# Kernel optimization log

Hardware: AMD Instinct MI355X
Metric: run time of the kernel (lower is better)

## Reference

```python
import jax, jax.numpy as jnp
import numpy as np

# ---- config (matches init_kwargs) ----
B, CIN, IMG = 4, 3, 129
PATCH, STRIDE, PAD = 4, 1, 1
DIM = CIN * PATCH * PATCH          # 48, Token_performer input dim
EMB = 256                          # out_channel -> in_dim -> emb
M = EMB // 2                       # kernel_ratio=0.5 random features
UP = 2                             # up_scale
EPS = 1e-8


def layernorm(x, g, b):
    mu = x.mean(-1, keepdims=True)
    var = ((x - mu) ** 2).mean(-1, keepdims=True)
    return (x - mu) / jnp.sqrt(var + 1e-5) * g + b


def unfold(x, k=PATCH, pad=PAD):
    # torch nn.Unfold, stride=1: output [B, C*k*k, L*L], channel order (c, kh, kw)
    Bs, C, H, W = x.shape
    xp = jnp.pad(x, ((0, 0), (0, 0), (pad, pad), (pad, pad)))
    L = H + 2 * pad - k + 1
    cols = jnp.stack([xp[:, :, i:i + L, j:j + L]
                      for i in range(k) for j in range(k)], axis=2)  # [B,C,k*k,L,L]
    return cols.reshape(Bs, C * k * k, L * L)


def prm_exp(x, w):
    # Performer positive random features: exp(w@x - |x|^2/2)/sqrt(m)
    xd = 0.5 * jnp.sum(x * x, axis=-1, keepdims=True)          # [B,T,1]
    wtx = jnp.einsum('btd,md->btm', x, w)                       # [B,T,M]
    return jnp.exp(wtx - xd) / jnp.sqrt(jnp.float32(w.shape[0]))


def upsample_bilinear_ac(x, scale):
    # nn.UpsamplingBilinear2d => align_corners=True
    Bs, C, H, W = x.shape
    Ho, Wo = H * scale, W * scale
    def coords(n_in, n_out):
        f = jnp.arange(n_out, dtype=jnp.float32) * (n_in - 1) / (n_out - 1)
        i0 = jnp.clip(jnp.floor(f).astype(jnp.int32), 0, n_in - 2)
        return i0, f - i0.astype(jnp.float32)
    h0, th = coords(H, Ho)
    w0, tw = coords(W, Wo)
    xh = x[:, :, h0, :] * (1 - th)[None, None, :, None] + x[:, :, h0 + 1, :] * th[None, None, :, None]
    return xh[:, :, :, w0] * (1 - tw) + xh[:, :, :, w0 + 1] * tw


def setup_inputs() -> dict:
    key = jax.random.key(0)
    ks = jax.random.split(key, 8)
    def n(k, shape, s=0.02):
        return jax.random.normal(k, shape, dtype=jnp.float32) * s
    return dict(
        x=jax.random.normal(ks[0], (B, CIN, IMG, IMG), dtype=jnp.float32),
        g1=jnp.ones((DIM,), jnp.float32), b1=jnp.zeros((DIM,), jnp.float32),
        w_kqv=n(ks[1], (DIM, 3 * EMB)), b_kqv=jnp.zeros((3 * EMB,), jnp.float32),
        w_prm=jax.random.normal(ks[2], (M, EMB), dtype=jnp.float32) * 0.7,  # ~ orthogonal*sqrt(m)
        w_proj=n(ks[3], (EMB, EMB)), b_proj=jnp.zeros((EMB,), jnp.float32),
        g2=jnp.ones((EMB,), jnp.float32), b2=jnp.zeros((EMB,), jnp.float32),
        w_mlp1=n(ks[4], (EMB, EMB)), b_mlp1=jnp.zeros((EMB,), jnp.float32),
        w_mlp2=n(ks[5], (EMB, EMB)), b_mlp2=jnp.zeros((EMB,), jnp.float32),
    )


def reference(x, g1, b1, w_kqv, b_kqv, w_prm, w_proj, b_proj, g2, b2,
              w_mlp1, b_mlp1, w_mlp2, b_mlp2):
    Bs = x.shape[0]
    t = unfold(x).transpose(0, 2, 1)                     # [B, T, DIM], T = 128*128
    h = layernorm(t, g1, b1)
    kqv = h @ w_kqv + b_kqv                              # [B, T, 3*EMB]
    k, q, v = jnp.split(kqv, 3, axis=-1)                 # torch split order: k, q, v
    kp, qp = prm_exp(k, w_prm), prm_exp(q, w_prm)        # [B, T, M]
    D = jnp.einsum('btm,bm->bt', qp, kp.sum(axis=1))[..., None]   # [B,T,1]
    kptv = jnp.einsum('btn,btm->bnm', v, kp)             # [B, EMB, M]
    y = jnp.einsum('btm,bnm->btn', qp, kptv) / (D + EPS) # [B, T, EMB]
    y = v + (y @ w_proj + b_proj)                        # skip uses v
    z = layernorm(y, g2, b2)
    y = y + (jax.nn.gelu(z @ w_mlp1 + b_mlp1, approximate=False) @ w_mlp2 + b_mlp2)
    T = y.shape[1]
    S = int(np.sqrt(T))
    img = y.transpose(0, 2, 1).reshape(Bs, EMB, S, S)    # [B, 256, 128, 128]
    return upsample_bilinear_ac(img, UP)                 # [B, 256, 256, 256]
```

## Files before the change

### kernel.cpp

```cpp
#include <hip/hip_runtime.h>
#include <math.h>

#define TOK   16384
#define DIM   48
#define EMB   256
#define MF    128
#define IMGsz 129

typedef __attribute__((ext_vector_type(8))) short    bf16x8;
typedef __attribute__((ext_vector_type(8))) unsigned short u16x8;
typedef __attribute__((ext_vector_type(4))) float    f32x4;

__device__ __forceinline__ ushort f2bf(float f) {
    union { float f; unsigned u; } v; v.f = f;
    unsigned u = v.u;
    return (ushort)((u + 0x7fffu + ((u >> 16) & 1u)) >> 16);
}
__device__ __forceinline__ float bf2f(ushort h) {
    union { unsigned u; float f; } v; v.u = ((unsigned)h) << 16; return v.f;
}

#define SWZ512(r,c) ((r)*512 + (((((c)>>3) ^ ((r)&7))) << 3) + ((c)&7))
#define SWZ64(r,c)  ((r)*64  + (((((c)>>3) ^ ((r)&7)) & 7) << 3) + ((c)&7))
#define SWZ256(r,c) ((r)*256 + (((((c)>>3) ^ ((r)&7))) << 3) + ((c)&7))

__device__ __forceinline__ int fragmajor(int n, int k, int KC) {
    return (((n >> 4)*KC + (k >> 5))*4 + ((k >> 3) & 3))*128 + (n & 15)*8 + (k & 7);
}

__global__ __launch_bounds__(256) void kprep(
    const float* __restrict__ w_kqv, const float* __restrict__ w_prm,
    const float* __restrict__ w_proj, const float* __restrict__ w_mlp1,
    const float* __restrict__ w_mlp2,
    ushort* __restrict__ wkqvT, ushort* __restrict__ wprm_bf, ushort* __restrict__ wT3)
{
    int blk = blockIdx.x, tid = threadIdx.x;
    if (blk < 768) {
        if (tid < 64) {
            float v = (tid < DIM) ? w_kqv[tid*768 + blk] : 0.f;
            wkqvT[fragmajor(blk, tid, 2)] = f2bf(v);
        }
    } else if (blk < 896) {
        int m = blk - 768;
        wprm_bf[fragmajor(m, tid, 8)] = f2bf(w_prm[m*256 + tid]);
    } else {
        int q = blk - 896;
        int w = q >> 8, n = q & 255;
        const float* src = (w == 0) ? w_proj : ((w == 1) ? w_mlp1 : w_mlp2);
        wT3[w*65536 + fragmajor(n, tid, 8)] = f2bf(src[tid*256 + n]);
    }
}

__global__ __launch_bounds__(256, 2) void k1_mfma(
    const float* __restrict__ x, const float* __restrict__ g1, const float* __restrict__ b1,
    const ushort* __restrict__ wkqvT, const float* __restrict__ b_kqv,
    const ushort* __restrict__ wprm_bf,
    ushort* __restrict__ vfrag_out, ushort* __restrict__ vT_out,
    ushort* __restrict__ kpT_out, ushort* __restrict__ qp_out)
{
    __shared__ __align__(16) ushort kq_bf[32*512];
    __shared__ __align__(16) ushort vt_bf[32*256];
    __shared__ float xdp[4][32][2];
    __shared__ float xd2[32][2];
    __shared__ float red1[32][8], red2[32][8];
    __shared__ float mu_s[32], iv_s[32];

    float*  t_s  = (float*)kq_bf;
    ushort* h_bf = vt_bf;

    const int blk = blockIdx.x;
    const int b  = blk >> 9;
    const int t0 = (blk & 511) << 5;
    const int tid = threadIdx.x;
    const int wid = tid >> 6;
    const int l15 = tid & 15, l4 = (tid >> 4) & 3;

    for (int e = tid; e < 32*DIM; e += 256) {
        int tok = e / DIM, j = e - tok*DIM;
        int t = t0 + tok;
        int lh = t >> 7, lw = t & 127;
        int c = j >> 4, kh = (j >> 2) & 3, kw = j & 3;
        int ih = lh + kh - 1, iw = lw + kw - 1;
        float val = 0.f;
        if (ih >= 0 && ih < IMGsz && iw >= 0 && iw < IMGsz)
            val = x[((b*3 + c)*IMGsz + ih)*IMGsz + iw];
        t_s[tok*DIM + j] = val;
    }
    __syncthreads();

    {
        int tg = tid >> 3, sl = tid & 7;
        const float* tr = &t_s[tg*DIM + sl*6];
        float s1 = 0.f, s2 = 0.f;
        #pragma unroll
        for (int j = 0; j < 6; j++) { float a = tr[j]; s1 += a; s2 = fmaf(a, a, s2); }
        red1[tg][sl] = s1; red2[tg][sl] = s2;
        __syncthreads();
        if (tid < 32) {
            float a = 0.f, q = 0.f;
            #pragma unroll
            for (int j = 0; j < 8; j++) { a += red1[tid][j]; q += red2[tid][j]; }
            float mu = a * (1.f/DIM);
            mu_s[tid] = mu;
            iv_s[tid] = rsqrtf(q*(1.f/DIM) - mu*mu + 1e-5f);
        }
        __syncthreads();
        float mu = mu_s[tg], iv = iv_s[tg];
        #pragma unroll
        for (int j = 0; j < 6; j++) {
            int c = sl*6 + j;
            h_bf[SWZ64(tg, c)] = f2bf((tr[j]-mu)*iv*g1[c] + b1[c]);
        }
        h_bf[SWZ64(tg, 48 + sl*2    )] = 0;
        h_bf[SWZ64(tg, 48 + sl*2 + 1)] = 0;
    }
    __syncthreads();

    f32x4 acc[2][12];
    #pragma unroll
    for (int m = 0; m < 2; m++)
        #pragma unroll
        for (int j = 0; j < 12; j++) { acc[m][j][0]=0.f; acc[m][j][1]=0.f; acc[m][j][2]=0.f; acc[m][j][3]=0.f; }
    #pragma unroll
    for (int kc = 0; kc < 2; kc++) {
        int ch = ((kc*4 + l4) ^ (l15 & 7)) << 3;
        bf16x8 a0 = *(const bf16x8*)&h_bf[ l15      *64 + ch];
        bf16x8 a1 = *(const bf16x8*)&h_bf[(16 + l15)*64 + ch];
        #pragma unroll
        for (int j = 0; j < 12; j++) {
            int ntile = wid + 4*j;
            bf16x8 bb = *(const bf16x8*)&wkqvT[(((ntile*2 + kc)*4 + l4)*16 + l15)*8];
            acc[0][j] = __builtin_amdgcn_mfma_f32_16x16x32_bf16(a0, bb, acc[0][j], 0, 0, 0);
            acc[1][j] = __builtin_amdgcn_mfma_f32_16x16x32_bf16(a1, bb, acc[1][j], 0, 0, 0);
        }
    }
    __syncthreads();

    {
        float pk[2][4], pq[2][4];
        #pragma unroll
        for (int m = 0; m < 2; m++)
            #pragma unroll
            for (int r = 0; r < 4; r++) { pk[m][r] = 0.f; pq[m][r] = 0.f; }
        #pragma unroll
        for (int j = 0; j < 12; j++) {
            int col = (wid + 4*j)*16 + l15;
            float bias = b_kqv[col];
            #pragma unroll
            for (int m = 0; m < 2; m++)
                #pragma unroll
                for (int r = 0; r < 4; r++) {
                    int row = m*16 + l4*4 + r;
                    float a = acc[m][j][r] + bias;
                    if (j < 4) {
                        pk[m][r] = fmaf(a, a, pk[m][r]);
                        kq_bf[SWZ512(row, col)] = f2bf(a);
                    } else if (j < 8) {
                        pq[m][r] = fmaf(a, a, pq[m][r]);
                        kq_bf[SWZ512(row, col)] = f2bf(a);
                    } else {
                        int n = col - 512;
                        vt_bf[row*256 + n] = f2bf(a);
                    }
                }
        }
        #pragma unroll
        for (int m = 0; m < 2; m++)
            #pragma unroll
            for (int r = 0; r < 4; r++) {
                float a = pk[m][r], q = pq[m][r];
                #pragma unroll
                for (int msk = 8; msk >= 1; msk >>= 1) {
                    a += __shfl_xor(a, msk);
                    q += __shfl_xor(q, msk);
                }
                if (l15 == 0) {
                    int row = m*16 + l4*4 + r;
                    xdp[wid][row][0] = a; xdp[wid][row][1] = q;
                }
            }
    }
    __syncthreads();
    if (tid < 64) {
        int row = tid >> 1, ty = tid & 1;
        xd2[row][ty] = 0.5f*(xdp[0][row][ty] + xdp[1][row][ty] + xdp[2][row][ty] + xdp[3][row][ty]);
    }

    {
        ushort* dst = vT_out + ((size_t)(b*EMB + tid))*TOK + t0;
        #pragma unroll
        for (int t8 = 0; t8 < 4; t8++) {
            u16x8 pk8;
            #pragma unroll
            for (int j = 0; j < 8; j++) pk8[j] = vt_bf[(t8*8 + j)*256 + tid];
            *(u16x8*)&dst[t8*8] = pk8;
        }
    }
    {
        u16x8 pk8[4];
        #pragma unroll
        for (int m = 0; m < 2; m++)
            #pragma unroll
            for (int nt = 0; nt < 4; nt++)
                #pragma unroll
                for (int r = 0; r < 4; r++) {
                    int row = m*16 + l4*4 + r;
                    int col = wid*64 + nt*16 + l15;
                    int idx = m*16 + nt*4 + r;
                    pk8[idx >> 3][idx & 7] = vt_bf[row*256 + col];
                }
        ushort* dst = vfrag_out + (size_t)blk*8192 + tid*32;
        #pragma unroll
        for (int i = 0; i < 4; i++) *(u16x8*)&dst[i*8] = pk8[i];
    }
    __syncthreads();

    f32x4 acc2[2][4];
    #pragma unroll
    for (int m = 0; m < 2; m++)
        #pragma unroll
        for (int n = 0; n < 4; n++) { acc2[m][n][0]=0.f; acc2[m][n][1]=0.f; acc2[m][n][2]=0.f; acc2[m][n][3]=0.f; }
    {
        const int cbase = (wid >= 2) ? 32 : 0;
        #pragma unroll
        for (int kc = 0; kc < 8; kc++) {
            int chunk = cbase + kc*4 + l4;
            int ch = (chunk ^ (l15 & 7)) << 3;
            bf16x8 a0 = *(const bf16x8*)&kq_bf[ l15      *512 + ch];
            bf16x8 a1 = *(const bf16x8*)&kq_bf[(16 + l15)*512 + ch];
            #pragma unroll
            for (int nt = 0; nt < 4; nt++) {
                int mtile = (wid & 1)*4 + nt;
                bf16x8 bb = *(const bf16x8*)&wprm_bf[(((mtile*8 + kc)*4 + l4)*16 + l15)*8];
                acc2[0][nt] = __builtin_amdgcn_mfma_f32_16x16x32_bf16(a0, bb, acc2[0][nt], 0, 0, 0);
                acc2[1][nt] = __builtin_amdgcn_mfma_f32_16x16x32_bf16(a1, bb, acc2[1][nt], 0, 0, 0);
            }
        }
    }

    {
        const float scale = 0.08838834764831845f;
        const bool isK = (wid < 2);
        #pragma unroll
        for (int m = 0; m < 2; m++)
            #pragma unroll
            for (int nt = 0; nt < 4; nt++) {
                #pragma unroll
                for (int r = 0; r < 4; r++) {
                    int row = m*16 + l4*4 + r;
                    int mcol = (wid & 1)*64 + nt*16 + l15;
                    float e = expf(acc2[m][nt][r] - xd2[row][isK ? 0 : 1]) * scale;
                    ushort bf = f2bf(e);
                    if (isK) vt_bf[row*256 + mcol] = bf;
                    else qp_out[(size_t)(b*TOK + t0 + row)*MF + mcol] = bf;
                }
            }
    }
    __syncthreads();

    if (tid < 128) {
        ushort* dst = kpT_out + ((size_t)(b*MF + tid))*TOK + t0;
        #pragma unroll
        for (int t8 = 0; t8 < 4; t8++) {
            u16x8 pk8;
            #pragma unroll
            for (int j = 0; j < 8; j++) pk8[j] = vt_bf[(t8*8 + j)*256 + tid];
            *(u16x8*)&dst[t8*8] = pk8;
        }
    }
}

__global__ __launch_bounds__(256) void k2_ksum(const ushort* __restrict__ kpT, float* __restrict__ ksum)
{
    __shared__ float red[4];
    int blk = blockIdx.x;
    int b = blk >> 7, m = blk & 127;
    int tid = threadIdx.x;
    const ushort* row = kpT + (size_t)(b*MF + m)*TOK;
    float s = 0.f;
    for (int i = tid; i < TOK/8; i += 256) {
        u16x8 v = *(const u16x8*)&row[i*8];
        #pragma unroll
        for (int j = 0; j < 8; j++) s += bf2f(v[j]);
    }
    #pragma unroll
    for (int msk = 32; msk >= 1; msk >>= 1) s += __shfl_xor(s, msk);
    if ((tid & 63) == 0) red[tid >> 6] = s;
    __syncthreads();
    if (tid == 0) ksum[b*MF + m] = red[0] + red[1] + red[2] + red[3];
}

__global__ __launch_bounds__(256) void k3_kptv_mfma(
    const ushort* __restrict__ vT, const ushort* __restrict__ kpT, float* __restrict__ part)
{
    int blk = blockIdx.x;
    int b = blk >> 6, ns = (blk >> 5) & 1, kc = blk & 31;
    const int tid = threadIdx.x;
    const int wid = tid >> 6;
    const int l15 = tid & 15, l4 = (tid >> 4) & 3;
    const int t0 = kc * 512;
    const int n0 = ns*128 + wid*32;

    f32x4 acc[2][8];
    #pragma unroll
    for (int m = 0; m < 2; m++)
        #pragma unroll
        for (int n = 0; n < 8; n++) { acc[m][n][0]=0.f; acc[m][n][1]=0.f; acc[m][n][2]=0.f; acc[m][n][3]=0.f; }

    #pragma unroll
    for (int ks = 0; ks < 16; ks++) {
        int k0 = t0 + ks*32 + l4*8;
        bf16x8 a0 = *(const bf16x8*)&vT[((size_t)(b*EMB + n0      + l15))*TOK + k0];
        bf16x8 a1 = *(const bf16x8*)&vT[((size_t)(b*EMB + n0 + 16 + l15))*TOK + k0];
        #pragma unroll
        for (int nt = 0; nt < 8; nt++) {
            bf16x8 bb = *(const bf16x8*)&kpT[((size_t)(b*MF + nt*16 + l15))*TOK + k0];
            acc[0][nt] = __builtin_amdgcn_mfma_f32_16x16x32_bf16(a0, bb, acc[0][nt], 0, 0, 0);
            acc[1][nt] = __builtin_amdgcn_mfma_f32_16x16x32_bf16(a1, bb, acc[1][nt], 0, 0, 0);
        }
    }
    #pragma unroll
    for (int mt = 0; mt < 2; mt++)
        #pragma unroll
        for (int nt = 0; nt < 8; nt++) {
            int n = n0 + mt*16 + l4*4;
            int m = nt*16 + l15;
            #pragma unroll
            for (int r = 0; r < 4; r++)
                part[(size_t)kc*131072 + (size_t)((b*EMB + n + r)*MF + m)] = acc[mt][nt][r];
        }
}

__global__ __launch_bounds__(256) void k3r_reduce(const float* __restrict__ part, float* __restrict__ kptv)
{
    int e = blockIdx.x*256 + threadIdx.x;
    float s = 0.f;
    #pragma unroll 8
    for (int kc = 0; kc < 32; kc++) s += part[(size_t)kc*131072 + e];
    kptv[e] = s;
}

__global__ __launch_bounds__(256) void k3c_combine(
    const float* __restrict__ kptv, const float* __restrict__ w_proj, ushort* __restrict__ C_bf)
{
    __shared__ float kp_s[256][8];
    int blk = blockIdx.x;
    int b = blk >> 4, m0 = (blk & 15)*8;
    int tid = threadIdx.x;

    #pragma unroll
    for (int pass = 0; pass < 8; pass++) {
        int n1 = pass*32 + (tid >> 3);
        kp_s[n1][tid & 7] = kptv[b*32768 + n1*128 + m0 + (tid & 7)];
    }
    __syncthreads();

    float acc[8];
    #pragma unroll
    for (int j = 0; j < 8; j++) acc[j] = 0.f;
    for (int n1 = 0; n1 < 256; n1++) {
        float w = w_proj[n1*256 + tid];
        #pragma unroll
        for (int j = 0; j < 8; j++) acc[j] = fmaf(kp_s[n1][j], w, acc[j]);
    }
    u16x8 pk;
    #pragma unroll
    for (int j = 0; j < 8; j++) pk[j] = f2bf(acc[j]);
    int base = (((tid >> 4)*4 + (m0 >> 5))*4 + ((m0 >> 3) & 3))*128 + (tid & 15)*8;
    *(u16x8*)&C_bf[b*32768 + base] = pk;
}

template<int K>
__device__ __forceinline__ void gemm32(const ushort* A_s, const ushort* __restrict__ B,
                                       f32x4 acc[2][4], int l15, int l4, int wid)
{
    __builtin_amdgcn_s_setprio(1);
    #pragma unroll
    for (int kc = 0; kc < (K >> 5); kc++) {
        const int ch = ((kc*4 + l4) ^ (l15 & 7)) << 3;
        bf16x8 a0 = *(const bf16x8*)&A_s[ l15      *256 + ch];
        bf16x8 a1 = *(const bf16x8*)&A_s[(16 + l15)*256 + ch];
        #pragma unroll
        for (int nt = 0; nt < 4; nt++) {
            int ntile = wid*4 + nt;
            bf16x8 bb = *(const bf16x8*)&B[(((ntile*(K >> 5) + kc)*4 + l4)*16 + l15)*8];
            acc[0][nt] = __builtin_amdgcn_mfma_f32_16x16x32_bf16(a0, bb, acc[0][nt], 0, 0, 0);
            acc[1][nt] = __builtin_amdgcn_mfma_f32_16x16x32_bf16(a1, bb, acc[1][nt], 0, 0, 0);
        }
    }
    __builtin_amdgcn_s_setprio(0);
}

__global__ __launch_bounds__(256, 4) void k4_attn_tail(
    const ushort* __restrict__ qp, const ushort* __restrict__ vfrag,
    const float* __restrict__ ksum, const ushort* __restrict__ C_bf,
    const ushort* __restrict__ wT,
    const float* __restrict__ b_proj,
    const float* __restrict__ g2, const float* __restrict__ b2,
    const float* __restrict__ b_mlp1, const float* __restrict__ b_mlp2,
    float* __restrict__ img2)
{
    __shared__ __align__(16) ushort A_s[16448];
    __shared__ float D_s[32];
    __shared__ float redD[32][8];
    __shared__ float red1[4][32], red2[4][32];
    __shared__ float mu_s[32], iv_s[32];

    const int blk = blockIdx.x;
    const int b  = blk >> 9;
    const int t0 = (blk & 511) << 5;
    const int tid = threadIdx.x;
    const int wid = tid >> 6;
    const int lane = tid & 63;
    const int l15 = lane & 15, l4 = lane >> 4;

    u16x8 vreg[4];
    {
        const ushort* vf = vfrag + (size_t)blk*8192 + tid*32;
        #pragma unroll
        for (int i = 0; i < 4; i++) vreg[i] = *(const u16x8*)&vf[i*8];
    }
    float bp[4];
    #pragma unroll
    for (int nt = 0; nt < 4; nt++) bp[nt] = b_proj[wid*64 + nt*16 + l15];

    {
        int tk = tid >> 3, seg = tid & 7;
        const ushort* qrow = qp + (size_t)(b*TOK + t0 + tk)*MF + seg*16;
        u16x8 q0 = *(const u16x8*)&qrow[0];
        u16x8 q1 = *(const u16x8*)&qrow[8];
        const float* ks = ksum + b*MF + seg*16;
        float dd = 0.f;
        #pragma unroll
        for (int j = 0; j < 8; j++) {
            dd = fmaf(bf2f(q0[j]), ks[j],   dd);
            dd = fmaf(bf2f(q1[j]), ks[j+8], dd);
        }
        redD[tk][seg] = dd;
        int xr = tk & 7;
        *(u16x8*)&A_s[tk*256 + (((seg*2  ) ^ xr) << 3)] = q0;
        *(u16x8*)&A_s[tk*256 + (((seg*2+1) ^ xr) << 3)] = q1;
    }
    __syncthreads();
    if (tid < 32) {
        float s = 0.f;
        #pragma unroll
        for (int j = 0; j < 8; j++) s += redD[tid][j];
        D_s[tid] = s + 1e-8f;
    }

    f32x4 acc[2][4];
    #define ZACC() { _Pragma("unroll") for (int m_=0;m_<2;m_++) _Pragma("unroll") for (int n_=0;n_<4;n_++) { acc[m_][n_][0]=0.f;acc[m_][n_][1]=0.f;acc[m_][n_][2]=0.f;acc[m_][n_][3]=0.f; } }

    ZACC();
    gemm32<MF>(A_s, C_bf + (size_t)b*32768, acc, l15, l4, wid);
    __syncthreads();
    float y2[2][4][4];
    #pragma unroll
    for (int nt = 0; nt < 4; nt++) {
        #pragma unroll
        for (int m = 0; m < 2; m++)
            #pragma unroll
            for (int r = 0; r < 4; r++) {
                int row = m*16 + l4*4 + r;
                int idx = m*16 + nt*4 + r;
                y2[m][nt][r] = acc[m][nt][r]/D_s[row] + bp[nt] + bf2f(vreg[idx >> 3][idx & 7]);
            }
    }

    {
        #pragma unroll
        for (int m = 0; m < 2; m++)
            #pragma unroll
            for (int r = 0; r < 4; r++) {
                float s1 = 0.f, s2 = 0.f;
                #pragma unroll
                for (int nt = 0; nt < 4; nt++) {
                    float a = y2[m][nt][r];
                    s1 += a; s2 = fmaf(a, a, s2);
                }
                #pragma unroll
                for (int msk = 8; msk >= 1; msk >>= 1) {
                    s1 += __shfl_xor(s1, msk);
                    s2 += __shfl_xor(s2, msk);
                }
                if (l15 == 0) {
                    int row = m*16 + l4*4 + r;
                    red1[wid][row] = s1; red2[wid][row] = s2;
                }
            }
        __syncthreads();
        if (tid < 32) {
            float a = red1[0][tid] + red1[1][tid] + red1[2][tid] + red1[3][tid];
            float q = red2[0][tid] + red2[1][tid] + red2[2][tid] + red2[3][tid];
            float mu = a * (1.f/EMB);
            mu_s[tid] = mu;
            iv_s[tid] = rsqrtf(q*(1.f/EMB) - mu*mu + 1e-5f);
        }
        __syncthreads();
        #pragma unroll
        for (int nt = 0; nt < 4; nt++) {
            int col = wid*64 + nt*16 + l15;
            float gg = g2[col], bb = b2[col];
            #pragma unroll
            for (int m = 0; m < 2; m++)
                #pragma unroll
                for (int r = 0; r < 4; r++) {
                    int row = m*16 + l4*4 + r;
                    A_s[SWZ256(row, col)] = f2bf((y2[m][nt][r] - mu_s[row])*iv_s[row]*gg + bb);
                }
        }
    }
    __syncthreads();

    ZACC();
    gemm32<EMB>(A_s, wT + 65536, acc, l15, l4, wid);
    __syncthreads();
    #pragma unroll
    for (int nt = 0; nt < 4; nt++) {
        int col = wid*64 + nt*16 + l15;
        float bm = b_mlp1[col];
        #pragma unroll
        for (int m = 0; m < 2; m++)
            #pragma unroll
            for (int r = 0; r < 4; r++) {
                int row = m*16 + l4*4 + r;
                float a = acc[m][nt][r] + bm;
                A_s[SWZ256(row, col)] = f2bf(0.5f*a*(1.f + erff(a*0.70710678118654752f)));
            }
    }
    __syncthreads();

    ZACC();
    gemm32<EMB>(A_s, wT + 131072, acc, l15, l4, wid);
    #pragma unroll
    for (int nt = 0; nt < 4; nt++) {
        int col = wid*64 + nt*16 + l15;
        float bm = b_mlp2[col];
        #pragma unroll
        for (int m = 0; m < 2; m++)
            #pragma unroll
            for (int r = 0; r < 4; r++)
                y2[m][nt][r] += acc[m][nt][r] + bm;
    }
    __syncthreads();

    float* A_f = (float*)A_s;
    #pragma unroll
    for (int nt = 0; nt < 4; nt++) {
        int col = wid*64 + nt*16 + l15;
        #pragma unroll
        for (int m = 0; m < 2; m++)
            #pragma unroll
            for (int r = 0; r < 4; r++)
                A_f[(m*16 + l4*4 + r)*257 + col] = y2[m][nt][r];
    }
    __syncthreads();
    {
        int tq = tid & 7, cb = tid >> 3;
        #pragma unroll
        for (int pass = 0; pass < 8; pass++) {
            int c = pass*32 + cb;
            f32x4 pk;
            #pragma unroll
            for (int j = 0; j < 4; j++) pk[j] = A_f[(tq*4 + j)*257 + c];
            *(f32x4*)&img2[((size_t)(b*EMB + c))*TOK + t0 + tq*4] = pk;
        }
    }
}

__global__ __launch_bounds__(256) void k6_upsample(const float* __restrict__ img2, float* __restrict__ out)
{
    int idx = blockIdx.x*256 + threadIdx.x;
    int wq = idx & 63;
    int ho = (idx >> 6) & 255;
    int c  = (idx >> 14) & 255;
    int b  = idx >> 22;
    const float sc = 127.f/255.f;
    float fh = ho * sc; int h0 = (int)fh; if (h0 > 126) h0 = 126; float th = fh - h0;
    int wo = wq*4;
    int w0[4]; float tw[4];
    #pragma unroll
    for (int j = 0; j < 4; j++) {
        float fw = (wo + j) * sc;
        int w = (int)fw; if (w > 126) w = 126;
        w0[j] = w; tw[j] = fw - w;
    }
    int wsrt = w0[0] > 124 ? 124 : w0[0];
    const float* p = img2 + (((size_t)(b*EMB + c))*128 + h0)*128 + wsrt;
    f32x4 r0 = *(const f32x4*)p;
    f32x4 r1 = *(const f32x4*)(p + 128);
    f32x4 o;
    #pragma unroll
    for (int j = 0; j < 4; j++) {
        int i = w0[j] - wsrt;
        float a00 = (i == 0) ? r0[0] : ((i == 1) ? r0[1] : r0[2]);
        float a01 = (i == 0) ? r0[1] : ((i == 1) ? r0[2] : r0[3]);
        float a10 = (i == 0) ? r1[0] : ((i == 1) ? r1[1] : r1[2]);
        float a11 = (i == 0) ? r1[1] : ((i == 1) ? r1[2] : r1[3]);
        float top = fmaf(a01 - a00, tw[j], a00);
        float bot = fmaf(a11 - a10, tw[j], a10);
        o[j] = fmaf(bot - top, th, top);
    }
    *(f32x4*)&out[(size_t)idx*4] = o;
}

extern "C" void kernel_launch(void* const* d_in, const int* in_sizes, int n_in,
                              void* d_out, int out_size, void* d_ws, size_t ws_size,
                              hipStream_t stream)
{
    const float* x      = (const float*)d_in[0];
    const float* g1     = (const float*)d_in[1];
    const float* b1     = (const float*)d_in[2];
    const float* w_kqv  = (const float*)d_in[3];
    const float* b_kqv  = (const float*)d_in[4];
    const float* w_prm  = (const float*)d_in[5];
    const float* w_proj = (const float*)d_in[6];
    const float* b_proj = (const float*)d_in[7];
    const float* g2     = (const float*)d_in[8];
    const float* b2     = (const float*)d_in[9];
    const float* w_mlp1 = (const float*)d_in[10];
    const float* b_mlp1 = (const float*)d_in[11];
    const float* w_mlp2 = (const float*)d_in[12];
    const float* b_mlp2 = (const float*)d_in[13];
    float* out = (float*)d_out;
    float* ws  = (float*)d_ws;

    ushort* vfrag    = (ushort*)(ws);
    ushort* qp_bf    = (ushort*)(ws + 8388608);
    ushort* vT_bf    = (ushort*)(ws + 12582912);
    ushort* kpT_bf   = (ushort*)(ws + 20971520);
    float*  img2     = ws + 12582912;
    float*  ksum     = ws + 29360128;
    ushort* wkqvT    = (ushort*)(ws + 29360640);
    ushort* wprm_bf  = (ushort*)(ws + 29385216);
    ushort* wT3      = (ushort*)(ws + 29401600);
    float*  kptv_f32 = ws + 29499904;
    ushort* C_bf     = (ushort*)(ws + 29630976);
    float*  part     = ws + 29696512;

    hipLaunchKernelGGL(kprep, dim3(1664), dim3(256), 0, stream,
                       w_kqv, w_prm, w_proj, w_mlp1, w_mlp2, wkqvT, wprm_bf, wT3);
    hipLaunchKernelGGL(k1_mfma, dim3(2048), dim3(256), 0, stream,
                       x, g1, b1, wkqvT, b_kqv, wprm_bf, vfrag, vT_bf, kpT_bf, qp_bf);
    hipLaunchKernelGGL(k2_ksum, dim3(512), dim3(256), 0, stream, kpT_bf, ksum);
    hipLaunchKernelGGL(k3_kptv_mfma, dim3(256), dim3(256), 0, stream, vT_bf, kpT_bf, part);
    hipLaunchKernelGGL(k3r_reduce, dim3(512), dim3(256), 0, stream, part, kptv_f32);
    hipLaunchKernelGGL(k3c_combine, dim3(64), dim3(256), 0, stream, kptv_f32, w_proj, C_bf);
    hipLaunchKernelGGL(k4_attn_tail, dim3(2048), dim3(256), 0, stream,
                       qp_bf, vfrag, ksum, C_bf, wT3, b_proj, g2, b2,
                       b_mlp1, b_mlp2, img2);
    hipLaunchKernelGGL(k6_upsample, dim3(65536), dim3(256), 0, stream, img2, out);
}
```

Baseline: 273.2 us.

## Fold random-feature projection into KQV weights and compute norms via Gram matrix

Precomputes w_kqv·w_prm^T for the k and q halves, plus a Gram matrix of the augmented k/q weights, in the prep kernel. The first kernel then runs one small GEMM over the 48-dim normalized input (with a constant-1 column for the bias) that yields v, the pre-exp random-feature logits and the squared-norm terms directly. This removes the separate 256-wide k/q intermediate and the second GEMM against w_prm, and cuts shared memory so occupancy can rise to 3 blocks per CU. In exchange, norms are computed as h^T G h in bf16, which may lose precision inside the exponent, and the prep kernel grows heavier dot-product work.

```diff
diff --git a/kernel.cpp b/kernel.cpp
--- a/kernel.cpp
+++ b/kernel.cpp
@@ -20,7 +20,6 @@
     union { unsigned u; float f; } v; v.u = ((unsigned)h) << 16; return v.f;
 }
 
-#define SWZ512(r,c) ((r)*512 + (((((c)>>3) ^ ((r)&7))) << 3) + ((c)&7))
 #define SWZ64(r,c)  ((r)*64  + (((((c)>>3) ^ ((r)&7)) & 7) << 3) + ((c)&7))
 #define SWZ256(r,c) ((r)*256 + (((((c)>>3) ^ ((r)&7))) << 3) + ((c)&7))
 
@@ -29,44 +28,76 @@
 }
 
 __global__ __launch_bounds__(256) void kprep(
-    const float* __restrict__ w_kqv, const float* __restrict__ w_prm,
-    const float* __restrict__ w_proj, const float* __restrict__ w_mlp1,
-    const float* __restrict__ w_mlp2,
-    ushort* __restrict__ wkqvT, ushort* __restrict__ wprm_bf, ushort* __restrict__ wT3)
-{
+    const float* __restrict__ w_kqv, const float* __restrict__ b_kqv,
+    const float* __restrict__ w_prm,
+    const float* __restrict__ w_mlp1, const float* __restrict__ w_mlp2,
+    ushort* __restrict__ Wbig, ushort* __restrict__ wT2, float* __restrict__ bkq)
+{
+    __shared__ float redp[64][4];
     int blk = blockIdx.x, tid = threadIdx.x;
-    if (blk < 768) {
+    if (blk < 256) {
         if (tid < 64) {
-            float v = (tid < DIM) ? w_kqv[tid*768 + blk] : 0.f;
-            wkqvT[fragmajor(blk, tid, 2)] = f2bf(v);
-        }
-    } else if (blk < 896) {
-        int m = blk - 768;
-        wprm_bf[fragmajor(m, tid, 8)] = f2bf(w_prm[m*256 + tid]);
+            float v = (tid < DIM) ? w_kqv[tid*768 + 512 + blk] : 0.f;
+            Wbig[fragmajor(blk, tid, 2)] = f2bf(v);
+        }
+    } else if (blk < 512) {
+        int isQ = (blk >= 384);
+        int m = blk - (isQ ? 384 : 256);
+        int d = tid & 63, part = tid >> 6;
+        float s = 0.f;
+        if (d < 48) {
+            const float* wr = w_kqv + d*768 + (isQ ? 256 : 0);
+            const float* pr = w_prm + m*256;
+            for (int n = part*64; n < part*64 + 64; n++) s += wr[n]*pr[n];
+        }
+        redp[d][part] = s;
+        __syncthreads();
+        if (tid < 64)
+            Wbig[fragmajor((isQ ? 384 : 256) + m, tid, 2)] =
+                f2bf(redp[tid][0]+redp[tid][1]+redp[tid][2]+redp[tid][3]);
+    } else if (blk < 640) {
+        int isQ = (blk >= 576);
+        int j = blk - (isQ ? 576 : 512);
+        int i = tid & 63, part = tid >> 6;
+        int off = isQ ? 256 : 0;
+        float s = 0.f;
+        for (int n = part*64; n < part*64 + 64; n++) {
+            float wi = (i < 48) ? w_kqv[i*768 + off + n] : (i == 48 ? b_kqv[off + n] : 0.f);
+            float wj = (j < 48) ? w_kqv[j*768 + off + n] : (j == 48 ? b_kqv[off + n] : 0.f);
+            s += wi*wj;
+        }
+        redp[i][part] = s;
+        __syncthreads();
+        if (tid < 64)
+            Wbig[fragmajor((isQ ? 576 : 512) + j, tid, 2)] =
+                f2bf(redp[tid][0]+redp[tid][1]+redp[tid][2]+redp[tid][3]);
+    } else if (blk < 1152) {
+        int w = (blk >= 896);
+        int n = blk - (w ? 896 : 640);
+        const float* src = w ? w_mlp2 : w_mlp1;
+        wT2[w*65536 + fragmajor(n, tid, 8)] = f2bf(src[tid*256 + n]);
     } else {
-        int q = blk - 896;
-        int w = q >> 8, n = q & 255;
-        const float* src = (w == 0) ? w_proj : ((w == 1) ? w_mlp1 : w_mlp2);
-        wT3[w*65536 + fragmajor(n, tid, 8)] = f2bf(src[tid*256 + n]);
-    }
-}
-
-__global__ __launch_bounds__(256, 2) void k1_mfma(
+        float s = 0.f;
+        int m = tid & 127, off = (tid >= 128) ? 256 : 0;
+        for (int n = 0; n < 256; n++) s += w_prm[m*256 + n]*b_kqv[off + n];
+        bkq[tid] = s;
+    }
+}
+
+__global__ __launch_bounds__(256, 3) void k1_mfma(
     const float* __restrict__ x, const float* __restrict__ g1, const float* __restrict__ b1,
-    const ushort* __restrict__ wkqvT, const float* __restrict__ b_kqv,
-    const ushort* __restrict__ wprm_bf,
+    const ushort* __restrict__ Wbig, const float* __restrict__ b_kqv,
+    const float* __restrict__ bkq,
     ushort* __restrict__ vfrag_out, ushort* __restrict__ vT_out,
     ushort* __restrict__ kpT_out, ushort* __restrict__ qp_out)
 {
-    __shared__ __align__(16) ushort kq_bf[32*512];
+    __shared__ __align__(16) ushort h_bf[32*64];
     __shared__ __align__(16) ushort vt_bf[32*256];
     __shared__ float xdp[4][32][2];
     __shared__ float xd2[32][2];
     __shared__ float red1[32][8], red2[32][8];
     __shared__ float mu_s[32], iv_s[32];
-
-    float*  t_s  = (float*)kq_bf;
-    ushort* h_bf = vt_bf;
+    float* t_s = (float*)vt_bf;
 
     const int blk = blockIdx.x;
     const int b  = blk >> 9;
@@ -106,80 +137,65 @@
         }
         __syncthreads();
         float mu = mu_s[tg], iv = iv_s[tg];
+        float hv[6];
+        #pragma unroll
+        for (int j = 0; j < 6; j++) hv[j] = (tr[j]-mu)*iv;
         #pragma unroll
         for (int j = 0; j < 6; j++) {
             int c = sl*6 + j;
-            h_bf[SWZ64(tg, c)] = f2bf((tr[j]-mu)*iv*g1[c] + b1[c]);
-        }
-        h_bf[SWZ64(tg, 48 + sl*2    )] = 0;
-        h_bf[SWZ64(tg, 48 + sl*2 + 1)] = 0;
-    }
-    __syncthreads();
-
-    f32x4 acc[2][12];
-    #pragma unroll
-    for (int m = 0; m < 2; m++)
-        #pragma unroll
-        for (int j = 0; j < 12; j++) { acc[m][j][0]=0.f; acc[m][j][1]=0.f; acc[m][j][2]=0.f; acc[m][j][3]=0.f; }
+            h_bf[SWZ64(tg, c)] = f2bf(hv[j]*g1[c] + b1[c]);
+        }
+        int c0 = 48 + sl*2;
+        h_bf[SWZ64(tg, c0    )] = (sl == 0) ? (ushort)0x3F80 : (ushort)0;
+        h_bf[SWZ64(tg, c0 + 1)] = 0;
+    }
+    __syncthreads();
+
+    f32x4 acc[10][2];
+    #pragma unroll
+    for (int j = 0; j < 10; j++)
+        #pragma unroll
+        for (int m = 0; m < 2; m++) { acc[j][m][0]=0.f; acc[j][m][1]=0.f; acc[j][m][2]=0.f; acc[j][m][3]=0.f; }
     #pragma unroll
     for (int kc = 0; kc < 2; kc++) {
         int ch = ((kc*4 + l4) ^ (l15 & 7)) << 3;
         bf16x8 a0 = *(const bf16x8*)&h_bf[ l15      *64 + ch];
         bf16x8 a1 = *(const bf16x8*)&h_bf[(16 + l15)*64 + ch];
         #pragma unroll
-        for (int j = 0; j < 12; j++) {
-            int ntile = wid + 4*j;
-            bf16x8 bb = *(const bf16x8*)&wkqvT[(((ntile*2 + kc)*4 + l4)*16 + l15)*8];
-            acc[0][j] = __builtin_amdgcn_mfma_f32_16x16x32_bf16(a0, bb, acc[0][j], 0, 0, 0);
-            acc[1][j] = __builtin_amdgcn_mfma_f32_16x16x32_bf16(a1, bb, acc[1][j], 0, 0, 0);
-        }
-    }
-    __syncthreads();
-
-    {
-        float pk[2][4], pq[2][4];
-        #pragma unroll
-        for (int m = 0; m < 2; m++)
-            #pragma unroll
-            for (int r = 0; r < 4; r++) { pk[m][r] = 0.f; pq[m][r] = 0.f; }
-        #pragma unroll
-        for (int j = 0; j < 12; j++) {
-            int col = (wid + 4*j)*16 + l15;
-            float bias = b_kqv[col];
-            #pragma unroll
-            for (int m = 0; m < 2; m++)
-                #pragma unroll
-                for (int r = 0; r < 4; r++) {
-                    int row = m*16 + l4*4 + r;
-                    float a = acc[m][j][r] + bias;
-                    if (j < 4) {
-                        pk[m][r] = fmaf(a, a, pk[m][r]);
-                        kq_bf[SWZ512(row, col)] = f2bf(a);
-                    } else if (j < 8) {
-                        pq[m][r] = fmaf(a, a, pq[m][r]);
-                        kq_bf[SWZ512(row, col)] = f2bf(a);
-                    } else {
-                        int n = col - 512;
-                        vt_bf[row*256 + n] = f2bf(a);
-                    }
-                }
-        }
+        for (int j = 0; j < 10; j++) {
+            int tile = wid + 4*j;
+            bf16x8 bb = *(const bf16x8*)&Wbig[(((tile*2 + kc)*4 + l4)*16 + l15)*8];
+            acc[j][0] = __builtin_amdgcn_mfma_f32_16x16x32_bf16(a0, bb, acc[j][0], 0, 0, 0);
+            acc[j][1] = __builtin_amdgcn_mfma_f32_16x16x32_bf16(a1, bb, acc[j][1], 0, 0, 0);
+        }
+    }
+
+    #pragma unroll
+    for (int j = 0; j < 4; j++) {
+        int col = (wid + 4*j)*16 + l15;
+        float bias = b_kqv[512 + col];
         #pragma unroll
         for (int m = 0; m < 2; m++)
             #pragma unroll
             for (int r = 0; r < 4; r++) {
-                float a = pk[m][r], q = pq[m][r];
-                #pragma unroll
-                for (int msk = 8; msk >= 1; msk >>= 1) {
-                    a += __shfl_xor(a, msk);
-                    q += __shfl_xor(q, msk);
-                }
-                if (l15 == 0) {
-                    int row = m*16 + l4*4 + r;
-                    xdp[wid][row][0] = a; xdp[wid][row][1] = q;
-                }
+                int row = m*16 + l4*4 + r;
+                vt_bf[row*256 + col] = f2bf(acc[j][m][r] + bias);
             }
     }
+    #pragma unroll
+    for (int m = 0; m < 2; m++)
+        #pragma unroll
+        for (int r = 0; r < 4; r++) {
+            int row = m*16 + l4*4 + r;
+            float hv = bf2f(h_bf[SWZ64(row, wid*16 + l15)]);
+            float sk = acc[8][m][r]*hv, sq = acc[9][m][r]*hv;
+            #pragma unroll
+            for (int msk = 8; msk >= 1; msk >>= 1) {
+                sk += __shfl_xor(sk, msk);
+                sq += __shfl_xor(sq, msk);
+            }
+            if (l15 == 0) { xdp[wid][row][0] = sk; xdp[wid][row][1] = sq; }
+        }
     __syncthreads();
     if (tid < 64) {
         int row = tid >> 1, ty = tid & 1;
@@ -215,45 +231,30 @@
     }
     __syncthreads();
 
-    f32x4 acc2[2][4];
-    #pragma unroll
-    for (int m = 0; m < 2; m++)
-        #pragma unroll
-        for (int n = 0; n < 4; n++) { acc2[m][n][0]=0.f; acc2[m][n][1]=0.f; acc2[m][n][2]=0.f; acc2[m][n][3]=0.f; }
-    {
-        const int cbase = (wid >= 2) ? 32 : 0;
-        #pragma unroll
-        for (int kc = 0; kc < 8; kc++) {
-            int chunk = cbase + kc*4 + l4;
-            int ch = (chunk ^ (l15 & 7)) << 3;
-            bf16x8 a0 = *(const bf16x8*)&kq_bf[ l15      *512 + ch];
-            bf16x8 a1 = *(const bf16x8*)&kq_bf[(16 + l15)*512 + ch];
-            #pragma unroll
-            for (int nt = 0; nt < 4; nt++) {
-                int mtile = (wid & 1)*4 + nt;
-                bf16x8 bb = *(const bf16x8*)&wprm_bf[(((mtile*8 + kc)*4 + l4)*16 + l15)*8];
-                acc2[0][nt] = __builtin_amdgcn_mfma_f32_16x16x32_bf16(a0, bb, acc2[0][nt], 0, 0, 0);
-                acc2[1][nt] = __builtin_amdgcn_mfma_f32_16x16x32_bf16(a1, bb, acc2[1][nt], 0, 0, 0);
+    const float scale = 0.08838834764831845f;
+    #pragma unroll
+    for (int j = 4; j < 6; j++) {
+        int mcol = (wid + 4*j)*16 + l15 - 256;
+        float bias = bkq[mcol];
+        #pragma unroll
+        for (int m = 0; m < 2; m++)
+            #pragma unroll
+            for (int r = 0; r < 4; r++) {
+                int row = m*16 + l4*4 + r;
+                vt_bf[row*256 + mcol] = f2bf(expf(acc[j][m][r] + bias - xd2[row][0]) * scale);
             }
-        }
-    }
-
-    {
-        const float scale = 0.08838834764831845f;
-        const bool isK = (wid < 2);
-        #pragma unroll
-        for (int m = 0; m < 2; m++)
-            #pragma unroll
-            for (int nt = 0; nt < 4; nt++) {
-                #pragma unroll
-                for (int r = 0; r < 4; r++) {
-                    int row = m*16 + l4*4 + r;
-                    int mcol = (wid & 1)*64 + nt*16 + l15;
-                    float e = expf(acc2[m][nt][r] - xd2[row][isK ? 0 : 1]) * scale;
-                    ushort bf = f2bf(e);
-                    if (isK) vt_bf[row*256 + mcol] = bf;
-                    else qp_out[(size_t)(b*TOK + t0 + row)*MF + mcol] = bf;
-                }
+    }
+    #pragma unroll
+    for (int j = 6; j < 8; j++) {
+        int mcol = (wid + 4*j)*16 + l15 - 384;
+        float bias = bkq[128 + mcol];
+        #pragma unroll
+        for (int m = 0; m < 2; m++)
+            #pragma unroll
+            for (int r = 0; r < 4; r++) {
+                int row = m*16 + l4*4 + r;
+                qp_out[(size_t)(b*TOK + t0 + row)*MF + mcol] =
+                    f2bf(expf(acc[j][m][r] + bias - xd2[row][1]) * scale);
             }
     }
     __syncthreads();
@@ -394,7 +395,7 @@
 __global__ __launch_bounds__(256, 4) void k4_attn_tail(
     const ushort* __restrict__ qp, const ushort* __restrict__ vfrag,
     const float* __restrict__ ksum, const ushort* __restrict__ C_bf,
-    const ushort* __restrict__ wT,
+    const ushort* __restrict__ wT2,
     const float* __restrict__ b_proj,
     const float* __restrict__ g2, const float* __restrict__ b2,
     const float* __restrict__ b_mlp1, const float* __restrict__ b_mlp2,
@@ -514,7 +515,7 @@
     __syncthreads();
 
     ZACC();
-    gemm32<EMB>(A_s, wT + 65536, acc, l15, l4, wid);
+    gemm32<EMB>(A_s, wT2, acc, l15, l4, wid);
     __syncthreads();
     #pragma unroll
     for (int nt = 0; nt < 4; nt++) {
@@ -532,7 +533,7 @@
     __syncthreads();
 
     ZACC();
-    gemm32<EMB>(A_s, wT + 131072, acc, l15, l4, wid);
+    gemm32<EMB>(A_s, wT2 + 65536, acc, l15, l4, wid);
     #pragma unroll
     for (int nt = 0; nt < 4; nt++) {
         int col = wid*64 + nt*16 + l15;
@@ -632,23 +633,23 @@
     ushort* kpT_bf   = (ushort*)(ws + 20971520);
     float*  img2     = ws + 12582912;
     float*  ksum     = ws + 29360128;
-    ushort* wkqvT    = (ushort*)(ws + 29360640);
-    ushort* wprm_bf  = (ushort*)(ws + 29385216);
-    ushort* wT3      = (ushort*)(ws + 29401600);
-    float*  kptv_f32 = ws + 29499904;
-    ushort* C_bf     = (ushort*)(ws + 29630976);
-    float*  part     = ws + 29696512;
-
-    hipLaunchKernelGGL(kprep, dim3(1664), dim3(256), 0, stream,
-                       w_kqv, w_prm, w_proj, w_mlp1, w_mlp2, wkqvT, wprm_bf, wT3);
+    ushort* Wbig     = (ushort*)(ws + 29360640);
+    ushort* wT2      = (ushort*)(ws + 29381120);
+    float*  bkq      = ws + 29446656;
+    float*  kptv_f32 = ws + 29446912;
+    ushort* C_bf     = (ushort*)(ws + 29577984);
+    float*  part     = ws + 29610752;
+
+    hipLaunchKernelGGL(kprep, dim3(1153), dim3(256), 0, stream,
+                       w_kqv, b_kqv, w_prm, w_mlp1, w_mlp2, Wbig, wT2, bkq);
     hipLaunchKernelGGL(k1_mfma, dim3(2048), dim3(256), 0, stream,
-                       x, g1, b1, wkqvT, b_kqv, wprm_bf, vfrag, vT_bf, kpT_bf, qp_bf);
+                       x, g1, b1, Wbig, b_kqv, bkq, vfrag, vT_bf, kpT_bf, qp_bf);
     hipLaunchKernelGGL(k2_ksum, dim3(512), dim3(256), 0, stream, kpT_bf, ksum);
     hipLaunchKernelGGL(k3_kptv_mfma, dim3(256), dim3(256), 0, stream, vT_bf, kpT_bf, part);
     hipLaunchKernelGGL(k3r_reduce, dim3(512), dim3(256), 0, stream, part, kptv_f32);
     hipLaunchKernelGGL(k3c_combine, dim3(64), dim3(256), 0, stream, kptv_f32, w_proj, C_bf);
     hipLaunchKernelGGL(k4_attn_tail, dim3(2048), dim3(256), 0, stream,
-                       qp_bf, vfrag, ksum, C_bf, wT3, b_proj, g2, b2,
+                       qp_bf, vfrag, ksum, C_bf, wT2, b_proj, g2, b2,
                        b_mlp1, b_mlp2, img2);
     hipLaunchKernelGGL(k6_upsample, dim3(65536), dim3(256), 0, stream, img2, out);
 }
```

Result: no change. 277.8 us (+1.7%).
